# Performance work log

Hardware: AMD Instinct MI355X
Metric: run time of the kernel (lower is better)

Reference implementation:

```python
import jax, jax.numpy as jnp
import numpy as np

VOCAB = 50000
EMBED = 256
HIDDEN = 512
H2 = HIDDEN // 2
TAGS = 32
START = 30
STOP = 31
B = 64
S = 512
NEG = -10000.0


def lstm_scan(x_sbe, h0, c0, wih, whh, bih, bhh, mask_sb):
    # x_sbe: [S,B,E]; masked (packed-sequence-equivalent) unidirectional LSTM.
    def step(carry, inp):
        h, c = carry
        xt, mt = inp
        gates = xt @ wih.T + h @ whh.T + (bih + bhh)  # [B,4*H2], gate order i,f,g,o
        i, f, g, o = jnp.split(gates, 4, axis=-1)
        c_new = jax.nn.sigmoid(f) * c + jax.nn.sigmoid(i) * jnp.tanh(g)
        h_new = jax.nn.sigmoid(o) * jnp.tanh(c_new)
        m = mt[:, None]
        return (jnp.where(m, h_new, h), jnp.where(m, c_new, c)), jnp.where(m, h_new, 0.0)
    _, outs = jax.lax.scan(step, (h0, c0), (x_sbe, mask_sb))
    return outs  # [S,B,H2]


def viterbi(feats, lengths, transitions):
    # feats: [B,S,T]; batched Viterbi with length masking (identity backpointers on pads).
    b, s, t = feats.shape
    init = jnp.full((b, t), NEG, feats.dtype).at[:, START].set(0.0)
    mask = jnp.arange(s)[None, :] < lengths[:, None]
    ident = jnp.arange(t)[None, :]

    def step(fv, inp):
        feat, m = inp
        scores = fv[:, None, :] + transitions[None, :, :]  # [B, next, prev]
        bp = jnp.argmax(scores, axis=-1)                   # [B,T]
        best = jnp.max(scores, axis=-1) + feat
        fv_new = jnp.where(m[:, None], best, fv)
        bp = jnp.where(m[:, None], bp, ident)
        return fv_new, bp

    fv, bps = jax.lax.scan(step, init, (feats.transpose(1, 0, 2), mask.T))
    terminal = fv + transitions[STOP][None, :]
    best_last = jnp.argmax(terminal, axis=-1)  # [B]
    path_score = jnp.take_along_axis(terminal, best_last[:, None], axis=1)[:, 0]

    def back(tag, bp):
        prev = jnp.take_along_axis(bp, tag[:, None], axis=1)[:, 0]
        return prev, tag

    _, path = jax.lax.scan(back, best_last, bps, reverse=True)  # path[t] = tag at step t
    return path_score, path.T  # [B], [B,S]


def setup_inputs() -> dict:
    key = jax.random.key(0)
    ks = jax.random.split(key, 18)
    sc_l = 1.0 / np.sqrt(H2)      # torch LSTM init U(-1/sqrt(H2), 1/sqrt(H2))
    sc_h = 1.0 / np.sqrt(HIDDEN)  # torch Linear init
    u = lambda k, sh, sc: jax.random.uniform(k, sh, jnp.float32, -sc, sc)
    inp = {
        'sentences': jax.random.randint(ks[0], (B, S), 0, VOCAB),
        'lengths': jax.random.randint(ks[1], (B,), S // 2, S + 1).astype(jnp.int32),
        'embedding': jax.random.normal(ks[2], (VOCAB, EMBED), jnp.float32),
        'wih_f': u(ks[3], (4 * H2, EMBED), sc_l),
        'whh_f': u(ks[4], (4 * H2, H2), sc_l),
        'bih_f': u(ks[5], (4 * H2,), sc_l),
        'bhh_f': u(ks[6], (4 * H2,), sc_l),
        'wih_b': u(ks[7], (4 * H2, EMBED), sc_l),
        'whh_b': u(ks[8], (4 * H2, H2), sc_l),
        'bih_b': u(ks[9], (4 * H2,), sc_l),
        'bhh_b': u(ks[10], (4 * H2,), sc_l),
        'w_h2t': u(ks[11], (TAGS, HIDDEN), sc_h),
        'b_h2t': u(ks[12], (TAGS,), sc_h),
        'h0': jax.random.normal(ks[14], (2, B, H2), jnp.float32),
        'c0': jax.random.normal(ks[15], (2, B, H2), jnp.float32),
    }
    trans = jax.random.normal(ks[13], (TAGS, TAGS), jnp.float32)
    inp['transitions'] = trans.at[START, :].set(NEG).at[:, STOP].set(NEG)
    return inp


def reference(sentences, lengths, embedding, wih_f, whh_f, bih_f, bhh_f, wih_b, whh_b, bih_b, bhh_b, w_h2t, b_h2t, transitions, h0, c0):
    emb = embedding[sentences]  # [B,S,E]
    pos = jnp.arange(S)[None, :]
    mask = pos < lengths[:, None]  # [B,S]
    # forward direction
    out_f = lstm_scan(emb.transpose(1, 0, 2), h0[0], c0[0], wih_f, whh_f, bih_f, bhh_f, mask.T)
    # backward direction: reverse each sequence within its own length
    rev_idx = jnp.where(mask, lengths[:, None] - 1 - pos, pos)  # involutive on valid region
    emb_rev = jnp.take_along_axis(emb, rev_idx[:, :, None], axis=1)
    out_b_rev = lstm_scan(emb_rev.transpose(1, 0, 2), h0[1], c0[1], wih_b, whh_b, bih_b, bhh_b, mask.T)
    out_b = jnp.take_along_axis(out_b_rev.transpose(1, 0, 2), rev_idx[:, :, None], axis=1)
    lstm_out = jnp.concatenate([out_f.transpose(1, 0, 2), out_b], axis=-1)  # [B,S,HIDDEN]
    feats = lstm_out @ w_h2t.T + b_h2t  # [B,S,TAGS]
    return viterbi(feats, lengths, transitions)
```

## Files before the change

### kernel.cpp

```cpp
#include <hip/hip_runtime.h>
#include <cstdio>
#include <cstdint>

typedef _Float16 h16;
typedef _Float16 half8 __attribute__((ext_vector_type(8)));
typedef _Float16 half4 __attribute__((ext_vector_type(4)));
typedef float floatx4 __attribute__((ext_vector_type(4)));

#define MFMA16(a, b, c) __builtin_amdgcn_mfma_f32_16x16x32_f16((a), (b), (c), 0, 0, 0)

static constexpr int NB = 64;
static constexpr int NS = 512;
static constexpr int NE = 256;
static constexpr int NH2 = 256;
static constexpr int NG = 1024;
static constexpr int TCH = 256;
static constexpr float LOSCL = 4096.0f;
static constexpr float LOINV = 0.000244140625f;

__device__ __forceinline__ float sigm(float x) { return 1.0f / (1.0f + __expf(-x)); }
__device__ __forceinline__ float tanha(float x) { return 1.0f - 2.0f / (1.0f + __expf(2.0f * x)); }

__global__ void k_prologue(const float* __restrict__ emb,
                           const float* __restrict__ wih_f, const float* __restrict__ wih_b,
                           const float* __restrict__ whh_f, const float* __restrict__ whh_b,
                           const float* __restrict__ w_h2t,
                           const float* __restrict__ bih_f, const float* __restrict__ bhh_f,
                           const float* __restrict__ bih_b, const float* __restrict__ bhh_b,
                           const int* __restrict__ sent, const int* __restrict__ lens,
                           h16* __restrict__ emb_hi, h16* __restrict__ emb_lo,
                           h16* __restrict__ wih_hi, h16* __restrict__ wih_lo,
                           h16* __restrict__ whh_hi, h16* __restrict__ whh_lo,
                           h16* __restrict__ wt_hi, h16* __restrict__ wt_lo,
                           float* __restrict__ bias, int* __restrict__ tok,
                           unsigned* __restrict__ ctr) {
  const int bx = blockIdx.x;
  const int tid = threadIdx.x;
  if (bx < 12500) {
    int i = bx * 256 + tid;
    float4 v = ((const float4*)emb)[i];
    float xs[4] = {v.x, v.y, v.z, v.w};
    half4 hv, lv;
#pragma unroll
    for (int k = 0; k < 4; ++k) {
      h16 h = (h16)xs[k];
      hv[k] = h;
      lv[k] = (h16)((xs[k] - (float)h) * LOSCL);
    }
    ((half4*)emb_hi)[i] = hv;
    ((half4*)emb_lo)[i] = lv;
    return;
  }
  if (bx < 13540) {
    int b2 = bx - 12500;
    const float* src;
    h16 *hi, *lo;
    int li;
    if (b2 < 256)       { src = wih_f; hi = wih_hi;          lo = wih_lo;          li = b2; }
    else if (b2 < 512)  { src = wih_b; hi = wih_hi + 262144; lo = wih_lo + 262144; li = b2 - 256; }
    else if (b2 < 768)  { src = whh_f; hi = whh_hi;          lo = whh_lo;          li = b2 - 512; }
    else if (b2 < 1024) { src = whh_b; hi = whh_hi + 262144; lo = whh_lo + 262144; li = b2 - 768; }
    else                { src = w_h2t; hi = wt_hi;           lo = wt_lo;           li = b2 - 1024; }
    int i = li * 256 + tid;
    float4 v = ((const float4*)src)[i];
    float xs[4] = {v.x, v.y, v.z, v.w};
    half4 hv, lv;
#pragma unroll
    for (int k = 0; k < 4; ++k) {
      h16 h = (h16)xs[k];
      hv[k] = h;
      lv[k] = (h16)((xs[k] - (float)h) * LOSCL);
    }
    ((half4*)hi)[i] = hv;
    ((half4*)lo)[i] = lv;
    return;
  }
  int idx = (bx - 13540) * 256 + tid;
  if (idx < 1024) ctr[idx] = 0u;
  if (idx < 2048) {
    const float* a = (idx < 1024) ? bih_f : bih_b;
    const float* b = (idx < 1024) ? bhh_f : bhh_b;
    int j = idx & 1023;
    bias[idx] = a[j] + b[j];
  }
  int q = idx - 2048;
  if (q >= 0 && q < 2 * NB * NS) {
    int d = q >> 15, r = q & 32767;
    int b = r >> 9, t = r & 511;
    int L = lens[b];
    int pos = (d == 0) ? t : ((t < L) ? (L - 1 - t) : t);
    tok[q] = sent[b * NS + pos];
  }
}

__launch_bounds__(512, 2)
__global__ void k_gemm(const h16* __restrict__ emb_hi, const h16* __restrict__ emb_lo,
                       const h16* __restrict__ wih_hi, const h16* __restrict__ wih_lo,
                       const int* __restrict__ tok, float* __restrict__ gates, int t0) {
  __shared__ h16 lA[2][128 * 64];
  __shared__ h16 lB[2][128 * 64];
  __shared__ int stok[128];

  const int bx = blockIdx.x;
  const int mb = bx & 127;
  const int nb = (bx >> 7) & 7;
  const int d = bx >> 10;
  const int tid = threadIdx.x;
  const int lane = tid & 63;
  const int w = tid >> 6;
  const int wmr = w >> 2;
  const int wnc = w & 3;

  if (tid < 128) {
    int row = mb * 128 + tid;
    int b = row & 63, tl = row >> 6;
    stok[tid] = tok[d * 32768 + b * 512 + (t0 + tl)];
  }
  __syncthreads();

  floatx4 accA[4][2], accB[4][2];
#pragma unroll
  for (int i = 0; i < 4; ++i)
#pragma unroll
    for (int j = 0; j < 2; ++j) { accA[i][j] = (floatx4)0.0f; accB[i][j] = (floatx4)0.0f; }

  auto stage = [&](int kc, int buf) {
    int rg = kc >> 2;
    int krb = (kc & 3) * 64;
    const h16* As = (rg == 1) ? emb_lo : emb_hi;
    const h16* Bs = ((rg == 2) ? wih_lo : wih_hi) + (size_t)d * NG * NE;
#pragma unroll
    for (int i = 0; i < 2; ++i) {
      int c = tid + i * 512;
      int row = c >> 3, x = c & 7, y = x ^ (row & 7);
      half8 va = *(const half8*)(As + (size_t)stok[row] * NE + krb + x * 8);
      *(half8*)&lA[buf][row * 64 + y * 8] = va;
    }
#pragma unroll
    for (int i = 0; i < 2; ++i) {
      int c = tid + i * 512;
      int row = c >> 3, x = c & 7, y = x ^ (row & 7);
      half8 vb = *(const half8*)(Bs + (size_t)(nb * 128 + row) * NE + krb + x * 8);
      *(half8*)&lB[buf][row * 64 + y * 8] = vb;
    }
  };

  stage(0, 0);
  int buf = 0;
  for (int kc = 0; kc < 12; ++kc) {
    __syncthreads();
    if (kc + 1 < 12) stage(kc + 1, buf ^ 1);
    int rg = kc >> 2;
#pragma unroll
    for (int ks = 0; ks < 2; ++ks) {
      half8 af[4], bf[2];
#pragma unroll
      for (int mt = 0; mt < 4; ++mt) {
        int r = wmr * 64 + mt * 16 + (lane & 15);
        int ch = ks * 4 + (lane >> 4);
        af[mt] = *(const half8*)&lA[buf][r * 64 + (ch ^ (r & 7)) * 8];
      }
#pragma unroll
      for (int nt = 0; nt < 2; ++nt) {
        int r = wnc * 32 + nt * 16 + (lane & 15);
        int ch = ks * 4 + (lane >> 4);
        bf[nt] = *(const half8*)&lB[buf][r * 64 + (ch ^ (r & 7)) * 8];
      }
      if (rg == 0) {
#pragma unroll
        for (int mt = 0; mt < 4; ++mt)
#pragma unroll
          for (int nt = 0; nt < 2; ++nt)
            accA[mt][nt] = MFMA16(af[mt], bf[nt], accA[mt][nt]);
      } else {
#pragma unroll
        for (int mt = 0; mt < 4; ++mt)
#pragma unroll
          for (int nt = 0; nt < 2; ++nt)
            accB[mt][nt] = MFMA16(af[mt], bf[nt], accB[mt][nt]);
      }
    }
    buf ^= 1;
  }
#pragma unroll
  for (int mt = 0; mt < 4; ++mt)
#pragma unroll
    for (int nt = 0; nt < 2; ++nt) {
      int col = nb * 128 + wnc * 32 + nt * 16 + (lane & 15);
#pragma unroll
      for (int q = 0; q < 4; ++q) {
        int mrow = mb * 128 + wmr * 64 + mt * 16 + (lane >> 4) * 4 + q;
        gates[((size_t)d * (TCH * 64) + mrow) * 1024 + col] =
            accA[mt][nt][q] + LOINV * accB[mt][nt][q];
      }
    }
}

__launch_bounds__(512, 2)
__global__ void k_recur(const h16* __restrict__ whh_hi, const h16* __restrict__ whh_lo,
                        const float* __restrict__ bias, const float* __restrict__ gates,
                        const int* __restrict__ lens, float* __restrict__ hst,
                        float* __restrict__ cst, uint64_t* h_ex, unsigned* ctr,
                        h16* __restrict__ ho_hi, h16* __restrict__ ho_lo,
                        int t0, int t1) {
  __shared__ h16 hAh[32 * 256];
  __shared__ h16 hAl[32 * 256];
  __shared__ float gbuf[32 * 68];

  const int bid = blockIdx.x;
  const int d = bid >> 5;
  const int hf = (bid >> 4) & 1;
  const int g = bid & 15;
  const int grp4 = d * 2 + hf;
  const int tid = threadIdx.x;
  const int lane = tid & 63;
  const int w = tid >> 6;
  const int wmr = w >> 2, wnc = w & 3;
  const int l15 = lane & 15, l4 = lane >> 4;

  const int j = wnc * 256 + g * 16 + l15;
  half8 bh[8], bl[8];
#pragma unroll
  for (int ks = 0; ks < 8; ++ks) {
    int k = ks * 32 + l4 * 8;
    bh[ks] = *(const half8*)(whh_hi + ((size_t)d * NG + j) * NE + k);
    bl[ks] = *(const half8*)(whh_lo + ((size_t)d * NG + j) * NE + k);
  }
  const float bias_r = bias[d * 1024 + j];

  const int cl = tid >> 4;
  const int u = tid & 15;
  const int chain = hf * 32 + cl;
  const int lenv = lens[chain];
  float creg = cst[((size_t)d * NB + chain) * NH2 + g * 16 + u];
  float hreg = hst[((size_t)d * NB + chain) * NH2 + g * 16 + u];

  const int cls0 = tid >> 6;
  const int ksb = (tid * 4) & 255;
  const int rr = wmr * 16 + l15;

  auto grpbase = [&](int phys) -> size_t {
    return ((size_t)(d * 4 + phys) * 64 + hf * 32) * 128;
  };
  unsigned* h32 = (unsigned*)h_ex;

  float gxp[4];
  auto load_gx = [&](int t, float gdst[4]) {
#pragma unroll
    for (int q = 0; q < 4; ++q) {
      int mrl = wmr * 16 + l4 * 4 + q;
      int chn = hf * 32 + mrl;
      gdst[q] = gates[((size_t)d * (TCH * 64) + (t - t0) * 64 + chn) * 1024 + j];
    }
  };
  load_gx(t0, gxp);

  for (int t = t0; t < t1; ++t) {
    if (t == t0) {
#pragma unroll
      for (int i = 0; i < 4; ++i) {
        int cls = cls0 + i * 8;
        float4 v = *(const float4*)(hst + ((size_t)d * NB + hf * 32 + cls) * NH2 + ksb);
        float xs[4] = {v.x, v.y, v.z, v.w};
        half4 hv, lv;
#pragma unroll
        for (int k = 0; k < 4; ++k) {
          h16 hh = (h16)xs[k];
          hv[k] = hh;
          lv[k] = (h16)((xs[k] - (float)hh) * LOSCL);
        }
        int ch = ksb >> 3, y = ch ^ (cls & 7);
        int off = cls * 256 + y * 8 + (ksb & 7);
        *(half4*)&hAh[off] = hv;
        *(half4*)&hAl[off] = lv;
      }
    } else {
      const uint64_t* src64 = h_ex + grpbase(t & 3);
      uint64_t va[8];
#pragma unroll
      for (int i = 0; i < 4; ++i) {
        va[2 * i] = __hip_atomic_load(src64 + tid * 2 + i * 1024, __ATOMIC_RELAXED,
                                      __HIP_MEMORY_SCOPE_AGENT);
        va[2 * i + 1] = __hip_atomic_load(src64 + tid * 2 + 1 + i * 1024, __ATOMIC_RELAXED,
                                          __HIP_MEMORY_SCOPE_AGENT);
      }
#pragma unroll
      for (int i = 0; i < 4; ++i) {
        int cls = cls0 + i * 8;
        uint64_t a = va[2 * i], b = va[2 * i + 1];
        unsigned us[4] = {(unsigned)a, (unsigned)(a >> 32), (unsigned)b, (unsigned)(b >> 32)};
        half4 hv, lv;
#pragma unroll
        for (int k = 0; k < 4; ++k) {
          hv[k] = __builtin_bit_cast(h16, (unsigned short)(us[k] & 0xffffu));
          lv[k] = __builtin_bit_cast(h16, (unsigned short)(us[k] >> 16));
        }
        int ch = ksb >> 3, y = ch ^ (cls & 7);
        int off = cls * 256 + y * 8 + (ksb & 7);
        *(half4*)&hAh[off] = hv;
        *(half4*)&hAl[off] = lv;
      }
    }
    __syncthreads();

    floatx4 aA = (floatx4)0.0f;
    floatx4 aB = (floatx4)0.0f;
#pragma unroll
    for (int ks = 0; ks < 8; ++ks) {
      int ch = ks * 4 + l4;
      int off = rr * 256 + (ch ^ (rr & 7)) * 8;
      half8 ah = *(const half8*)&hAh[off];
      half8 al = *(const half8*)&hAl[off];
      aA = MFMA16(ah, bh[ks], aA);
      aB = MFMA16(ah, bl[ks], aB);
      aB = MFMA16(al, bh[ks], aB);
    }
    {
      int jn = wnc * 16 + l15;
#pragma unroll
      for (int q = 0; q < 4; ++q) {
        int mrl = wmr * 16 + l4 * 4 + q;
        gbuf[mrl * 68 + jn] = aA[q] + LOINV * aB[q] + gxp[q] + bias_r;
      }
    }
    __syncthreads();

    const bool mk = (t < lenv);
    float hw;
    unsigned wd;
    {
      float ig = gbuf[cl * 68 + u];
      float fg = gbuf[cl * 68 + 16 + u];
      float gg = gbuf[cl * 68 + 32 + u];
      float og = gbuf[cl * 68 + 48 + u];
      float cn = sigm(fg) * creg + sigm(ig) * tanha(gg);
      float hn = sigm(og) * tanha(cn);
      if (mk) { creg = cn; hreg = hn; }
      hw = mk ? hn : 0.0f;
      h16 ph = (h16)hreg;
      h16 pl = (h16)((hreg - (float)ph) * LOSCL);
      wd = (unsigned)__builtin_bit_cast(unsigned short, ph) |
           ((unsigned)__builtin_bit_cast(unsigned short, pl) << 16);
    }
    if (t < t1 - 1) {
      size_t si = (((size_t)(d * 4 + ((t + 1) & 3)) * 64 + chain) * 256) + g * 16 + u;
      __hip_atomic_store(h32 + si, wd, __ATOMIC_RELAXED, __HIP_MEMORY_SCOPE_AGENT);
      __syncthreads();
      if (tid == 0)
        __hip_atomic_store(&ctr[(grp4 * 16 + g) * 16], (unsigned)(t + 1), __ATOMIC_RELAXED,
                           __HIP_MEMORY_SCOPE_AGENT);
    }

    {
      int pos = (d == 0) ? t : (mk ? (lenv - 1 - t) : t);
      size_t hoff = ((size_t)chain * NS + pos) * 512 + d * 256 + (size_t)(g * 16 + u);
      h16 a = (h16)hw;
      ho_hi[hoff] = a;
      ho_lo[hoff] = (h16)((hw - (float)a) * LOSCL);
    }
    if (t + 1 < t1) load_gx(t + 1, gxp);

    if (t < t1 - 1) {
      if (tid < 16) {
        unsigned want = (unsigned)(t + 1);
        while (__hip_atomic_load(&ctr[(grp4 * 16 + tid) * 16], __ATOMIC_RELAXED,
                                 __HIP_MEMORY_SCOPE_AGENT) < want)
          __builtin_amdgcn_s_sleep(1);
      }
      __syncthreads();
    }
  }

  cst[((size_t)d * NB + chain) * NH2 + g * 16 + u] = creg;
  hst[((size_t)d * NB + chain) * NH2 + g * 16 + u] = hreg;
}

__launch_bounds__(512, 2)
__global__ void k_featsg(const h16* __restrict__ A_hi, const h16* __restrict__ A_lo,
                         const h16* __restrict__ wt_hi, const h16* __restrict__ wt_lo,
                         const float* __restrict__ bt, float* __restrict__ feats) {
  __shared__ h16 lA[2][128 * 64];
  __shared__ h16 lB[2][32 * 64];
  const int mb = blockIdx.x;
  const int tid = threadIdx.x, lane = tid & 63, w = tid >> 6;

  floatx4 accA[2], accB[2];
  accA[0] = accA[1] = (floatx4)0.0f;
  accB[0] = accB[1] = (floatx4)0.0f;

  auto stage = [&](int kc, int buf) {
    int rg = kc >> 3;
    int krb = (kc & 7) * 64;
    const h16* As = (rg == 1) ? A_lo : A_hi;
    const h16* Bs = (rg == 2) ? wt_lo : wt_hi;
#pragma unroll
    for (int i = 0; i < 2; ++i) {
      int c = tid + i * 512;
      int row = c >> 3, x = c & 7, y = x ^ (row & 7);
      half8 v = *(const half8*)(As + (size_t)(mb * 128 + row) * 512 + krb + x * 8);
      *(half8*)&lA[buf][row * 64 + y * 8] = v;
    }
    if (tid < 256) {
      int row = tid >> 3, x = tid & 7, y = x ^ (row & 7);
      half8 v = *(const half8*)(Bs + (size_t)row * 512 + krb + x * 8);
      *(half8*)&lB[buf][row * 64 + y * 8] = v;
    }
  };

  stage(0, 0);
  int buf = 0;
  for (int kc = 0; kc < 24; ++kc) {
    __syncthreads();
    if (kc + 1 < 24) stage(kc + 1, buf ^ 1);
    int rg = kc >> 3;
#pragma unroll
    for (int ks = 0; ks < 2; ++ks) {
      int rA = w * 16 + (lane & 15);
      int ch = ks * 4 + (lane >> 4);
      half8 a = *(const half8*)&lA[buf][rA * 64 + (ch ^ (rA & 7)) * 8];
#pragma unroll
      for (int nt = 0; nt < 2; ++nt) {
        int rB = nt * 16 + (lane & 15);
        half8 b = *(const half8*)&lB[buf][rB * 64 + (ch ^ (rB & 7)) * 8];
        if (rg == 0) accA[nt] = MFMA16(a, b, accA[nt]);
        else         accB[nt] = MFMA16(a, b, accB[nt]);
      }
    }
    buf ^= 1;
  }
#pragma unroll
  for (int nt = 0; nt < 2; ++nt) {
    int col = nt * 16 + (lane & 15);
    float bv = bt[col];
#pragma unroll
    for (int q = 0; q < 4; ++q) {
      int mr = mb * 128 + w * 16 + (lane >> 4) * 4 + q;
      feats[(size_t)mr * 32 + col] = accA[nt][q] + LOINV * accB[nt][q] + bv;
    }
  }
}

__global__ void k_viterbi(const float* __restrict__ feats, const int* __restrict__ lens,
                          const float* __restrict__ trans, float* __restrict__ out) {
  __shared__ float TL[32 * 33];
  __shared__ float fv[2][32];
  __shared__ unsigned char bp[512][32];
  __shared__ unsigned char pth[512];
  __shared__ float sc_sh;

  const int b = blockIdx.x;
  const int tid = threadIdx.x;
  const int L = lens[b];
  const int j = tid & 31, hfx = tid >> 5;

  for (int i = tid; i < 1024; i += 64) {
    int ii = i >> 5, jj = i & 31;
    TL[ii * 33 + jj] = trans[jj * 32 + ii];
  }
  if (tid < 32) fv[0][tid] = (tid == 30) ? 0.0f : -10000.0f;
  __syncthreads();

  const float* fb = feats + (size_t)b * 512 * 32;
  float ftn = fb[j];
  for (int t = 0; t < L; ++t) {
    float ft = ftn;
    if (t + 1 < L) ftn = fb[(t + 1) * 32 + j];
    const float* fcur = fv[t & 1];
    int i0 = hfx * 16;
    float best = fcur[i0] + TL[i0 * 33 + j];
    int bi = i0;
#pragma unroll
    for (int ii = 1; ii < 16; ++ii) {
      int i = i0 + ii;
      float v = fcur[i] + TL[i * 33 + j];
      if (v > best) { best = v; bi = i; }
    }
    float ob = __shfl_xor(best, 32);
    int obi = __shfl_xor(bi, 32);
    if (hfx == 0) {
      if (ob > best) { best = ob; bi = obi; }
      bp[t][j] = (unsigned char)bi;
      fv[(t + 1) & 1][j] = best + ft;
    }
    __syncthreads();
  }
  if (tid == 0) {
    const float* fvf = fv[L & 1];
    float bsc = fvf[0] + TL[0 * 33 + 31];
    int bl = 0;
    for (int i = 1; i < 32; ++i) {
      float v = fvf[i] + TL[i * 33 + 31];
      if (v > bsc) { bsc = v; bl = i; }
    }
    sc_sh = bsc;
    int tag = bl;
    for (int t = 511; t >= 0; --t) {
      pth[t] = (unsigned char)tag;
      if (t < L) tag = bp[t][tag];
    }
  }
  __syncthreads();
  for (int t = tid; t < 512; t += 64) out[64 + (size_t)b * 512 + t] = (float)pth[t];
  if (tid == 0) out[b] = sc_sh;
}

extern "C" void kernel_launch(void* const* d_in, const int* in_sizes, int n_in,
                              void* d_out, int out_size, void* d_ws, size_t ws_size,
                              hipStream_t stream) {
  (void)in_sizes; (void)n_in; (void)out_size;
  const int* sent = (const int*)d_in[0];
  const int* lens = (const int*)d_in[1];
  const float* emb = (const float*)d_in[2];
  const float* wih_f = (const float*)d_in[3];
  const float* whh_f = (const float*)d_in[4];
  const float* bih_f = (const float*)d_in[5];
  const float* bhh_f = (const float*)d_in[6];
  const float* wih_b = (const float*)d_in[7];
  const float* whh_b = (const float*)d_in[8];
  const float* bih_b = (const float*)d_in[9];
  const float* bhh_b = (const float*)d_in[10];
  const float* w_h2t = (const float*)d_in[11];
  const float* b_h2t = (const float*)d_in[12];
  const float* h0 = (const float*)d_in[13];
  const float* c0 = (const float*)d_in[14];
  const float* trans = (const float*)d_in[15];
  float* out = (float*)d_out;

  char* base = (char*)d_ws;
  size_t off = 0;
  auto alloc = [&](size_t bytes) -> void* {
    void* r = base + off;
    off = (off + bytes + 255) & ~(size_t)255;
    return r;
  };
  h16* emb_hi = (h16*)alloc(50000 * 256 * 2);
  h16* emb_lo = (h16*)alloc(50000 * 256 * 2);
  h16* wih_hi = (h16*)alloc(2 * 1024 * 256 * 2);
  h16* wih_lo = (h16*)alloc(2 * 1024 * 256 * 2);
  h16* whh_hi = (h16*)alloc(2 * 1024 * 256 * 2);
  h16* whh_lo = (h16*)alloc(2 * 1024 * 256 * 2);
  h16* wt_hi = (h16*)alloc(32 * 512 * 2);
  h16* wt_lo = (h16*)alloc(32 * 512 * 2);
  float* bias = (float*)alloc(2 * 1024 * 4);
  int* tok = (int*)alloc(2 * 64 * 512 * 4);
  uint64_t* h_ex = (uint64_t*)alloc(2 * 4 * 64 * 256 * 4);
  unsigned* ctr = (unsigned*)alloc(1024 * 4);
  float* hst = (float*)alloc(2 * 64 * 256 * 4);
  float* cst = (float*)alloc(2 * 64 * 256 * 4);
  float* feats = (float*)alloc((size_t)64 * 512 * 32 * 4);
  h16* ho_hi = (h16*)alloc((size_t)64 * 512 * 512 * 2);
  h16* ho_lo = (h16*)alloc((size_t)64 * 512 * 512 * 2);
  float* gates = (float*)alloc((size_t)2 * TCH * 64 * 1024 * 4);

  if (off > ws_size) {
    fprintf(stderr, "kernel_launch: need %zu ws bytes, have %zu\n", off, ws_size);
    return;
  }

  k_prologue<<<13804, 256, 0, stream>>>(emb, wih_f, wih_b, whh_f, whh_b, w_h2t,
                                        bih_f, bhh_f, bih_b, bhh_b, sent, lens,
                                        emb_hi, emb_lo, wih_hi, wih_lo, whh_hi, whh_lo,
                                        wt_hi, wt_lo, bias, tok, ctr);
  hipMemcpyAsync(hst, h0, 2 * 64 * 256 * 4, hipMemcpyDeviceToDevice, stream);
  hipMemcpyAsync(cst, c0, 2 * 64 * 256 * 4, hipMemcpyDeviceToDevice, stream);

  for (int chunk = 0; chunk < 2; ++chunk) {
    int t0 = chunk * TCH, t1 = t0 + TCH;
    k_gemm<<<2048, 512, 0, stream>>>(emb_hi, emb_lo, wih_hi, wih_lo, tok, gates, t0);
    k_recur<<<64, 512, 0, stream>>>(whh_hi, whh_lo, bias, gates, lens, hst, cst, h_ex,
                                    ctr, ho_hi, ho_lo, t0, t1);
  }
  k_featsg<<<256, 512, 0, stream>>>(ho_hi, ho_lo, wt_hi, wt_lo, b_h2t, feats);
  k_viterbi<<<64, 64, 0, stream>>>(feats, lens, trans, out);
}
```

Before: 1.816 ms.

## Split recurrent LSTM kernel over 128 blocks with K-split across wave groups

The persistent recurrence kernel now launches 128 blocks, each handling 16 batch chains instead of 32. The two wave groups inside a block split the hidden-dimension K reduction and combine partial sums through shared memory, rather than splitting rows. The aim is to halve the per-step serial MFMA and exchange work per block and to use more CUs on the latency-bound recurrence. In exchange there are more sync groups and counters, an extra partial-sum reduction, and half the threads idle in the elementwise gate phase.

```diff
diff --git a/kernel.cpp b/kernel.cpp
--- a/kernel.cpp
+++ b/kernel.cpp
@@ -76,7 +76,7 @@
     return;
   }
   int idx = (bx - 13540) * 256 + tid;
-  if (idx < 1024) ctr[idx] = 0u;
+  if (idx < 2048) ctr[idx] = 0u;
   if (idx < 2048) {
     const float* a = (idx < 1024) ? bih_f : bih_b;
     const float* b = (idx < 1024) ? bhh_f : bhh_b;
@@ -203,44 +203,47 @@
                         float* __restrict__ cst, uint64_t* h_ex, unsigned* ctr,
                         h16* __restrict__ ho_hi, h16* __restrict__ ho_lo,
                         int t0, int t1) {
-  __shared__ h16 hAh[32 * 256];
-  __shared__ h16 hAl[32 * 256];
-  __shared__ float gbuf[32 * 68];
+  __shared__ h16 hAh[16 * 256];
+  __shared__ h16 hAl[16 * 256];
+  __shared__ float gbuf[2 * 16 * 68];
 
   const int bid = blockIdx.x;
-  const int d = bid >> 5;
-  const int hf = (bid >> 4) & 1;
+  const int d = bid >> 6;
+  const int q4 = (bid >> 4) & 3;
   const int g = bid & 15;
-  const int grp4 = d * 2 + hf;
+  const int gamma = d * 4 + q4;
   const int tid = threadIdx.x;
   const int lane = tid & 63;
   const int w = tid >> 6;
-  const int wmr = w >> 2, wnc = w & 3;
+  const int wk = w >> 2;
+  const int wnc = w & 3;
   const int l15 = lane & 15, l4 = lane >> 4;
 
   const int j = wnc * 256 + g * 16 + l15;
-  half8 bh[8], bl[8];
-#pragma unroll
-  for (int ks = 0; ks < 8; ++ks) {
-    int k = ks * 32 + l4 * 8;
+  half8 bh[4], bl[4];
+#pragma unroll
+  for (int ks = 0; ks < 4; ++ks) {
+    int k = (wk * 4 + ks) * 32 + l4 * 8;
     bh[ks] = *(const half8*)(whh_hi + ((size_t)d * NG + j) * NE + k);
     bl[ks] = *(const half8*)(whh_lo + ((size_t)d * NG + j) * NE + k);
   }
   const float bias_r = bias[d * 1024 + j];
 
-  const int cl = tid >> 4;
+  const int cl = (tid >> 4) & 15;
   const int u = tid & 15;
-  const int chain = hf * 32 + cl;
+  const int chain = q4 * 16 + cl;
   const int lenv = lens[chain];
-  float creg = cst[((size_t)d * NB + chain) * NH2 + g * 16 + u];
-  float hreg = hst[((size_t)d * NB + chain) * NH2 + g * 16 + u];
+  float creg = 0.0f, hreg = 0.0f;
+  if (tid < 256) {
+    creg = cst[((size_t)d * NB + chain) * NH2 + g * 16 + u];
+    hreg = hst[((size_t)d * NB + chain) * NH2 + g * 16 + u];
+  }
 
   const int cls0 = tid >> 6;
   const int ksb = (tid * 4) & 255;
-  const int rr = wmr * 16 + l15;
 
   auto grpbase = [&](int phys) -> size_t {
-    return ((size_t)(d * 4 + phys) * 64 + hf * 32) * 128;
+    return ((size_t)(d * 4 + phys) * 64 + q4 * 16) * 128;
   };
   unsigned* h32 = (unsigned*)h_ex;
 
@@ -248,19 +251,19 @@
   auto load_gx = [&](int t, float gdst[4]) {
 #pragma unroll
     for (int q = 0; q < 4; ++q) {
-      int mrl = wmr * 16 + l4 * 4 + q;
-      int chn = hf * 32 + mrl;
+      int mrl = l4 * 4 + q;
+      int chn = q4 * 16 + mrl;
       gdst[q] = gates[((size_t)d * (TCH * 64) + (t - t0) * 64 + chn) * 1024 + j];
     }
   };
-  load_gx(t0, gxp);
+  if (wk == 0) load_gx(t0, gxp);
 
   for (int t = t0; t < t1; ++t) {
     if (t == t0) {
 #pragma unroll
-      for (int i = 0; i < 4; ++i) {
+      for (int i = 0; i < 2; ++i) {
         int cls = cls0 + i * 8;
-        float4 v = *(const float4*)(hst + ((size_t)d * NB + hf * 32 + cls) * NH2 + ksb);
+        float4 v = *(const float4*)(hst + ((size_t)d * NB + q4 * 16 + cls) * NH2 + ksb);
         float xs[4] = {v.x, v.y, v.z, v.w};
         half4 hv, lv;
 #pragma unroll
@@ -276,16 +279,16 @@
       }
     } else {
       const uint64_t* src64 = h_ex + grpbase(t & 3);
-      uint64_t va[8];
-#pragma unroll
-      for (int i = 0; i < 4; ++i) {
+      uint64_t va[4];
+#pragma unroll
+      for (int i = 0; i < 2; ++i) {
         va[2 * i] = __hip_atomic_load(src64 + tid * 2 + i * 1024, __ATOMIC_RELAXED,
                                       __HIP_MEMORY_SCOPE_AGENT);
         va[2 * i + 1] = __hip_atomic_load(src64 + tid * 2 + 1 + i * 1024, __ATOMIC_RELAXED,
                                           __HIP_MEMORY_SCOPE_AGENT);
       }
 #pragma unroll
-      for (int i = 0; i < 4; ++i) {
+      for (int i = 0; i < 2; ++i) {
         int cls = cls0 + i * 8;
         uint64_t a = va[2 * i], b = va[2 * i + 1];
         unsigned us[4] = {(unsigned)a, (unsigned)(a >> 32), (unsigned)b, (unsigned)(b >> 32)};
@@ -306,9 +309,9 @@
     floatx4 aA = (floatx4)0.0f;
     floatx4 aB = (floatx4)0.0f;
 #pragma unroll
-    for (int ks = 0; ks < 8; ++ks) {
-      int ch = ks * 4 + l4;
-      int off = rr * 256 + (ch ^ (rr & 7)) * 8;
+    for (int ks = 0; ks < 4; ++ks) {
+      int ch = (wk * 4 + ks) * 4 + l4;
+      int off = l15 * 256 + ((ch ^ (l15 & 7)) * 8);
       half8 ah = *(const half8*)&hAh[off];
       half8 al = *(const half8*)&hAl[off];
       aA = MFMA16(ah, bh[ks], aA);
@@ -319,20 +322,22 @@
       int jn = wnc * 16 + l15;
 #pragma unroll
       for (int q = 0; q < 4; ++q) {
-        int mrl = wmr * 16 + l4 * 4 + q;
-        gbuf[mrl * 68 + jn] = aA[q] + LOINV * aB[q] + gxp[q] + bias_r;
+        int mrl = l4 * 4 + q;
+        float v = aA[q] + LOINV * aB[q];
+        if (wk == 0) v += gxp[q] + bias_r;
+        gbuf[(wk * 16 + mrl) * 68 + jn] = v;
       }
     }
     __syncthreads();
 
     const bool mk = (t < lenv);
-    float hw;
-    unsigned wd;
-    {
-      float ig = gbuf[cl * 68 + u];
-      float fg = gbuf[cl * 68 + 16 + u];
-      float gg = gbuf[cl * 68 + 32 + u];
-      float og = gbuf[cl * 68 + 48 + u];
+    float hw = 0.0f;
+    unsigned wd = 0;
+    if (tid < 256) {
+      float ig = gbuf[cl * 68 + u]        + gbuf[(16 + cl) * 68 + u];
+      float fg = gbuf[cl * 68 + 16 + u]   + gbuf[(16 + cl) * 68 + 16 + u];
+      float gg = gbuf[cl * 68 + 32 + u]   + gbuf[(16 + cl) * 68 + 32 + u];
+      float og = gbuf[cl * 68 + 48 + u]   + gbuf[(16 + cl) * 68 + 48 + u];
       float cn = sigm(fg) * creg + sigm(ig) * tanha(gg);
       float hn = sigm(og) * tanha(cn);
       if (mk) { creg = cn; hreg = hn; }
@@ -343,27 +348,29 @@
            ((unsigned)__builtin_bit_cast(unsigned short, pl) << 16);
     }
     if (t < t1 - 1) {
-      size_t si = (((size_t)(d * 4 + ((t + 1) & 3)) * 64 + chain) * 256) + g * 16 + u;
-      __hip_atomic_store(h32 + si, wd, __ATOMIC_RELAXED, __HIP_MEMORY_SCOPE_AGENT);
+      if (tid < 256) {
+        size_t si = (((size_t)(d * 4 + ((t + 1) & 3)) * 64 + chain) * 256) + g * 16 + u;
+        __hip_atomic_store(h32 + si, wd, __ATOMIC_RELAXED, __HIP_MEMORY_SCOPE_AGENT);
+      }
       __syncthreads();
       if (tid == 0)
-        __hip_atomic_store(&ctr[(grp4 * 16 + g) * 16], (unsigned)(t + 1), __ATOMIC_RELAXED,
+        __hip_atomic_store(&ctr[(gamma * 16 + g) * 16], (unsigned)(t + 1), __ATOMIC_RELAXED,
                            __HIP_MEMORY_SCOPE_AGENT);
     }
 
-    {
+    if (tid < 256) {
       int pos = (d == 0) ? t : (mk ? (lenv - 1 - t) : t);
       size_t hoff = ((size_t)chain * NS + pos) * 512 + d * 256 + (size_t)(g * 16 + u);
       h16 a = (h16)hw;
       ho_hi[hoff] = a;
       ho_lo[hoff] = (h16)((hw - (float)a) * LOSCL);
     }
-    if (t + 1 < t1) load_gx(t + 1, gxp);
+    if (wk == 0 && t + 1 < t1) load_gx(t + 1, gxp);
 
     if (t < t1 - 1) {
       if (tid < 16) {
         unsigned want = (unsigned)(t + 1);
-        while (__hip_atomic_load(&ctr[(grp4 * 16 + tid) * 16], __ATOMIC_RELAXED,
+        while (__hip_atomic_load(&ctr[(gamma * 16 + tid) * 16], __ATOMIC_RELAXED,
                                  __HIP_MEMORY_SCOPE_AGENT) < want)
           __builtin_amdgcn_s_sleep(1);
       }
@@ -371,8 +378,10 @@
     }
   }
 
-  cst[((size_t)d * NB + chain) * NH2 + g * 16 + u] = creg;
-  hst[((size_t)d * NB + chain) * NH2 + g * 16 + u] = hreg;
+  if (tid < 256) {
+    cst[((size_t)d * NB + chain) * NH2 + g * 16 + u] = creg;
+    hst[((size_t)d * NB + chain) * NH2 + g * 16 + u] = hreg;
+  }
 }
 
 __launch_bounds__(512, 2)
@@ -544,7 +553,7 @@
   float* bias = (float*)alloc(2 * 1024 * 4);
   int* tok = (int*)alloc(2 * 64 * 512 * 4);
   uint64_t* h_ex = (uint64_t*)alloc(2 * 4 * 64 * 256 * 4);
-  unsigned* ctr = (unsigned*)alloc(1024 * 4);
+  unsigned* ctr = (unsigned*)alloc(2048 * 4);
   float* hst = (float*)alloc(2 * 64 * 256 * 4);
   float* cst = (float*)alloc(2 * 64 * 256 * 4);
   float* feats = (float*)alloc((size_t)64 * 512 * 32 * 4);
@@ -567,8 +576,8 @@
   for (int chunk = 0; chunk < 2; ++chunk) {
     int t0 = chunk * TCH, t1 = t0 + TCH;
     k_gemm<<<2048, 512, 0, stream>>>(emb_hi, emb_lo, wih_hi, wih_lo, tok, gates, t0);
-    k_recur<<<64, 512, 0, stream>>>(whh_hi, whh_lo, bias, gates, lens, hst, cst, h_ex,
-                                    ctr, ho_hi, ho_lo, t0, t1);
+    k_recur<<<128, 512, 0, stream>>>(whh_hi, whh_lo, bias, gates, lens, hst, cst, h_ex,
+                                     ctr, ho_hi, ho_lo, t0, t1);
   }
   k_featsg<<<256, 512, 0, stream>>>(ho_hi, ho_lo, wt_hi, wt_lo, b_h2t, feats);
   k_viterbi<<<64, 64, 0, stream>>>(feats, lens, trans, out);
```

New measurement: 1.534 ms. 15.5% less time.
